# Kernel tuning notes

Hardware: AMD Instinct MI355X
Metric: run time of the kernel (lower is better)

Reference implementation:

```python
import jax, jax.numpy as jnp
import numpy as np

B, N, C, H = 16, 4096, 256, 4
D = C // H

def setup_inputs() -> dict:
    key = jax.random.key(0)
    ks = jax.random.split(key, 8)
    w = 0.01  # small init, mimics xavier_uniform gain=0.1
    x = jax.random.normal(ks[0], (B, N, C), jnp.float32)
    S = jax.random.normal(ks[1], (B, H, D, D), jnp.float32) * 0.1
    Wq = jax.random.normal(ks[2], (C, C), jnp.float32) * w
    Wk = jax.random.normal(ks[3], (C, C), jnp.float32) * w
    Wv = jax.random.normal(ks[4], (C, C), jnp.float32) * w
    Wb = jax.random.normal(ks[5], (H, C), jnp.float32) * w  # beta_proj (zeros in torch init; random for nontrivial math)
    Wo = jax.random.normal(ks[6], (C, C), jnp.float32) * w
    g_rms = jnp.ones((C,), jnp.float32)
    return {"x": x, "S": S, "Wq": Wq, "Wk": Wk, "Wv": Wv, "Wb": Wb, "Wo": Wo, "g_rms": g_rms}

def reference(x, S, Wq, Wk, Wv, Wb, Wo, g_rms):
    b, n, c = x.shape
    h = Wb.shape[0]
    d = c // h
    # projections -> (B,H,N,D)
    q = (x @ Wq.T).reshape(b, n, h, d).transpose(0, 2, 1, 3)
    k = (x @ Wk.T).reshape(b, n, h, d).transpose(0, 2, 1, 3)
    v = (x @ Wv.T).reshape(b, n, h, d).transpose(0, 2, 1, 3)
    # feature map + L2 normalize keys
    k = jax.nn.elu(k) + 1.0
    k = k / (jnp.linalg.norm(k, axis=-1, keepdims=True) + 1e-6)
    # per-head gates (B,H,N,1)
    beta = jax.nn.sigmoid(jnp.einsum('bnc,hc->bhn', x, Wb))[..., None]
    # decay + state read
    Sd = S * 0.95
    y = jnp.einsum('bhij,bhnj->bhni', Sd, q)
    pred = jnp.einsum('bhij,bhnj->bhni', Sd, k)
    # delta-rule write: outer(mean weighted error, mean key)
    w_err = jnp.mean(beta * (v - pred), axis=2)  # (B,H,D)
    w_key = jnp.mean(k, axis=2)                  # (B,H,D)
    S_new = jnp.clip(Sd + jnp.einsum('bhi,bhj->bhij', w_err, w_key), -10.0, 10.0)
    # merge heads, RMSNorm, output projection
    y = y.transpose(0, 2, 1, 3).reshape(b, n, c)
    y = y * jax.lax.rsqrt(jnp.mean(y * y, axis=-1, keepdims=True) + 1e-6) * g_rms
    out = y @ Wo.T
    return out, S_new
```

## Files before the change

kernel.cpp:

```cpp
#include <hip/hip_runtime.h>
#include <math.h>


typedef _Float16 f16;
typedef f16 f16x8 __attribute__((ext_vector_type(8)));
typedef f16 f16x4 __attribute__((ext_vector_type(4)));
typedef float f32x4 __attribute__((ext_vector_type(4)));

typedef const __attribute__((address_space(1))) void gvoid;
typedef __attribute__((address_space(3))) void svoid;

__device__ __forceinline__ void gload16(const void* g, void* l) {
  __builtin_amdgcn_global_load_lds((gvoid*)g, (svoid*)l, 16, 0, 0);
}

__device__ __forceinline__ f16x8 cvt8(const float* q) {
  float4 a = *(const float4*)q;
  float4 b = *(const float4*)(q + 4);
  f16x8 r;
  r[0] = (f16)a.x; r[1] = (f16)a.y; r[2] = (f16)a.z; r[3] = (f16)a.w;
  r[4] = (f16)b.x; r[5] = (f16)b.y; r[6] = (f16)b.z; r[7] = (f16)b.w;
  return r;
}

__global__ __launch_bounds__(256) void prep_w(
    const float* __restrict__ Wk, const float* __restrict__ Wo,
    const float* __restrict__ g, f16* __restrict__ Wkh,
    f16* __restrict__ Wogh) {
  int i = blockIdx.x * 256 + threadIdx.x;
#pragma unroll
  for (int j = 0; j < 4; ++j) {
    int idx = i + j * 16384;
    Wkh[idx] = (f16)Wk[idx];
    Wogh[idx] = (f16)(Wo[idx] * g[idx & 255]);
  }
}

__global__ __launch_bounds__(256) void beta_xbsum_h(
    const float* __restrict__ x, const float* __restrict__ Wb,
    float* __restrict__ betaArr, float* __restrict__ xbsum,
    f16* __restrict__ xh) {
  const int t = threadIdx.x;
  const int wave = t >> 6, lane = t & 63;
  const int b = blockIdx.x >> 6;
  const int tile = blockIdx.x & 63;
  float4 wb[4];
#pragma unroll
  for (int h = 0; h < 4; ++h) wb[h] = *(const float4*)(Wb + h * 256 + lane * 4);
  float xacc[4][4] = {};
  const size_t rowbase = (size_t)b * 4096 + tile * 64;
  __shared__ float bsh[4][64];
  float4 xv = *(const float4*)(x + (rowbase + wave) * 256 + lane * 4);
#pragma unroll 2
  for (int i = 0; i < 16; ++i) {
    int r = i * 4 + wave;
    float4 nx = xv;
    if (i < 15)
      nx = *(const float4*)(x + (rowbase + r + 4) * 256 + lane * 4);
    f16x4 hx;
    hx[0] = (f16)xv.x; hx[1] = (f16)xv.y; hx[2] = (f16)xv.z; hx[3] = (f16)xv.w;
    *(f16x4*)(xh + (rowbase + r) * 256 + lane * 4) = hx;
#pragma unroll
    for (int h = 0; h < 4; ++h) {
      float s = xv.x * wb[h].x + xv.y * wb[h].y + xv.z * wb[h].z + xv.w * wb[h].w;
#pragma unroll
      for (int off = 32; off; off >>= 1) s += __shfl_xor(s, off);
      float bh = 1.f / (1.f + __expf(-s));
      if (lane == h) bsh[h][r] = bh;
      xacc[h][0] += bh * xv.x; xacc[h][1] += bh * xv.y;
      xacc[h][2] += bh * xv.z; xacc[h][3] += bh * xv.w;
    }
    xv = nx;
  }
  __shared__ float xbp[4][4][256];
#pragma unroll
  for (int h = 0; h < 4; ++h)
#pragma unroll
    for (int j = 0; j < 4; ++j) xbp[wave][h][lane * 4 + j] = xacc[h][j];
  __syncthreads();
  {
    int h = t >> 6, r = t & 63;
    betaArr[((size_t)(b * 4 + h) << 12) + tile * 64 + r] = bsh[h][r];
  }
  for (int idx = t; idx < 1024; idx += 256) {
    int h = idx >> 8, c = idx & 255;
    float s = xbp[0][h][c] + xbp[1][h][c] + xbp[2][h][c] + xbp[3][h][c];
    atomicAdd(&xbsum[(b * 4 + h) * 256 + c], s);
  }
}

__global__ __launch_bounds__(256) void kgemm_h(
    const f16* __restrict__ xh, const f16* __restrict__ Wkh,
    const float* __restrict__ betaArr,
    float* __restrict__ ksum, float* __restrict__ kbsum) {
  __shared__ union {
    struct { f16 A[128][64]; f16 B[128][64]; } s;
    f16 K[128][128];
  } u;
  __shared__ float bstage[2][128];
  const int t = threadIdx.x;
  const int m0 = blockIdx.y * 128;
  const int n0 = blockIdx.x * 128;
  const int b = m0 >> 12;
  const int wave = t >> 6, lane = t & 63;
  const int wm = (wave >> 1) * 64, wn = (wave & 1) * 64;
  const int fr = lane & 15, fq = lane >> 4;
  const int fr7 = fr & 7;
  const int srow = lane >> 3;
  const int sc = (lane & 7) ^ srow;
  {
    int hh = t >> 7, r = t & 127;
    bstage[hh][r] =
        betaArr[((size_t)(b * 4 + (n0 >> 6) + hh) << 12) + (m0 & 4095) + r];
  }
  const char* Ab = (const char*)&u.s.A[0][0];
  const char* Bb = (const char*)&u.s.B[0][0];
  f32x4 acc[4][4] = {};
#pragma unroll 1
  for (int kt = 0; kt < 4; ++kt) {
    const int k0 = kt * 64;
#pragma unroll
    for (int j = 0; j < 4; ++j) {
      int c = j * 4 + wave;
      int row = c * 8 + srow;
      gload16(xh + (size_t)(m0 + row) * 256 + k0 + sc * 8, &u.s.A[0][0] + c * 512);
      gload16(Wkh + (size_t)(n0 + row) * 256 + k0 + sc * 8, &u.s.B[0][0] + c * 512);
    }
    __syncthreads();
#pragma unroll
    for (int ks = 0; ks < 2; ++ks) {
      const int p = ((ks * 4 + fq) ^ fr7) << 4;
      f16x8 afr[4], bfr[4];
#pragma unroll
      for (int mi = 0; mi < 4; ++mi)
        afr[mi] = *(const f16x8*)(Ab + (wm + mi * 16 + fr) * 128 + p);
#pragma unroll
      for (int ni = 0; ni < 4; ++ni)
        bfr[ni] = *(const f16x8*)(Bb + (wn + ni * 16 + fr) * 128 + p);
#pragma unroll
      for (int mi = 0; mi < 4; ++mi)
#pragma unroll
        for (int ni = 0; ni < 4; ++ni)
          acc[mi][ni] = __builtin_amdgcn_mfma_f32_16x16x32_f16(
              afr[mi], bfr[ni], acc[mi][ni], 0, 0, 0);
    }
    __syncthreads();
  }
#pragma unroll
  for (int mi = 0; mi < 4; ++mi)
#pragma unroll
    for (int rr = 0; rr < 4; ++rr) {
      float s = 0.f;
#pragma unroll
      for (int ni = 0; ni < 4; ++ni) {
        float v = acc[mi][ni][rr];
        v = v > 0.f ? v + 1.f : __expf(v);
        acc[mi][ni][rr] = v;
        s += v * v;
      }
#pragma unroll
      for (int off = 1; off < 16; off <<= 1) s += __shfl_xor(s, off);
      float inv = 1.f / (sqrtf(s) + 1e-6f);
#pragma unroll
      for (int ni = 0; ni < 4; ++ni) acc[mi][ni][rr] *= inv;
    }
#pragma unroll
  for (int mi = 0; mi < 4; ++mi)
#pragma unroll
    for (int ni = 0; ni < 4; ++ni)
#pragma unroll
      for (int rr = 0; rr < 4; ++rr)
        u.K[wm + mi * 16 + fq * 4 + rr][wn + ni * 16 + fr] = (f16)acc[mi][ni][rr];
  __syncthreads();
  if (t < 128) {
    const int c = t, hl = c >> 6;
    float sk = 0.f, skb = 0.f;
#pragma unroll 4
    for (int r = 0; r < 128; ++r) {
      float v = (float)u.K[r][c];
      float be = bstage[hl][r];
      sk += v;
      skb += be * v;
    }
    int gh = b * 4 + (n0 >> 6) + hl;
    atomicAdd(&ksum[gh * 64 + (c & 63)], sk);
    atomicAdd(&kbsum[gh * 64 + (c & 63)], skb);
  }
}

__global__ __launch_bounds__(256) void fold_M(
    const float* __restrict__ S, const float* __restrict__ Wq,
    f16* __restrict__ M) {
  const int bh = blockIdx.y;
  const int dq = blockIdx.x;
  const int h = bh & 3;
  const int t = threadIdx.x;
  const float* Sp = S + (size_t)bh * 4096 + dq * 8 * 64;
  const float* Wp = Wq + (size_t)h * 64 * 256 + t;
  float m[8] = {};
#pragma unroll 4
  for (int e = 0; e < 64; ++e) {
    float wv = Wp[e * 256];
#pragma unroll
    for (int dd = 0; dd < 8; ++dd) m[dd] += Sp[dd * 64 + e] * wv;
  }
  f16* Mb = M + (size_t)(bh >> 2) * 65536;
#pragma unroll
  for (int dd = 0; dd < 8; ++dd)
    Mb[(size_t)(h * 64 + dq * 8 + dd) * 256 + t] = (f16)(0.95f * m[dd]);
}

__global__ __launch_bounds__(256) void yogemm_h(
    const f16* __restrict__ xh, const f16* __restrict__ M,
    const f16* __restrict__ Wogh, float* __restrict__ out) {
  __shared__ f16 Bst[256 * 64];
  __shared__ f16 Ast[64 * 64];
  __shared__ f16 yl[64 * 256];
  __shared__ float ssq[4][64];
  __shared__ float rs_l[64];
  const int t = threadIdx.x;
  const int m0 = blockIdx.x * 64;
  const int b = m0 >> 12;
  const f16* Mb = M + (size_t)b * 65536;
  const int wave = t >> 6, lane = t & 63;
  const int wn = wave * 64;
  const int fr = lane & 15, fq = lane >> 4;
  const int fr7 = fr & 7;
  const int srow = lane >> 3;
  const int sc = (lane & 7) ^ srow;
  const char* Ab = (const char*)Ast;
  const char* Bb = (const char*)Bst;
  f32x4 acc[4][4] = {};
#pragma unroll 1
  for (int kt = 0; kt < 4; ++kt) {
    const int k0 = kt * 64;
    if (wave < 2) {
      int c = wave * 4 + (lane >> 4);
      int l16 = lane & 15;
    }
#pragma unroll
    for (int j = 0; j < 2; ++j) {
      int c = j * 4 + wave;
      int row = c * 8 + srow;
      gload16(xh + (size_t)(m0 + row) * 256 + k0 + sc * 8, Ast + c * 512);
    }
#pragma unroll
    for (int j = 0; j < 8; ++j) {
      int c = j * 4 + wave;
      int row = c * 8 + srow;
      gload16(Mb + (size_t)row * 256 + k0 + sc * 8, Bst + c * 512);
    }
    __syncthreads();
#pragma unroll
    for (int ks = 0; ks < 2; ++ks) {
      const int p = ((ks * 4 + fq) ^ fr7) << 4;
      f16x8 afr[4], bfr[4];
#pragma unroll
      for (int mi = 0; mi < 4; ++mi)
        afr[mi] = *(const f16x8*)(Ab + (mi * 16 + fr) * 128 + p);
#pragma unroll
      for (int ni = 0; ni < 4; ++ni)
        bfr[ni] = *(const f16x8*)(Bb + (wn + ni * 16 + fr) * 128 + p);
#pragma unroll
      for (int mi = 0; mi < 4; ++mi)
#pragma unroll
        for (int ni = 0; ni < 4; ++ni)
          acc[mi][ni] = __builtin_amdgcn_mfma_f32_16x16x32_f16(
              afr[mi], bfr[ni], acc[mi][ni], 0, 0, 0);
    }
    __syncthreads();
  }
#pragma unroll
  for (int mi = 0; mi < 4; ++mi)
#pragma unroll
    for (int rr = 0; rr < 4; ++rr) {
      float s = 0.f;
#pragma unroll
      for (int ni = 0; ni < 4; ++ni) {
        float v = acc[mi][ni][rr];
        s += v * v;
      }
#pragma unroll
      for (int off = 1; off < 16; off <<= 1) s += __shfl_xor(s, off);
      if (fr == 0) ssq[wave][mi * 16 + fq * 4 + rr] = s;
    }
  __syncthreads();
  if (t < 64)
    rs_l[t] = rsqrtf((ssq[0][t] + ssq[1][t] + ssq[2][t] + ssq[3][t]) *
                         (1.f / 256.f) +
                     1e-6f);
  __syncthreads();
#pragma unroll
  for (int mi = 0; mi < 4; ++mi)
#pragma unroll
    for (int rr = 0; rr < 4; ++rr) {
      int row = mi * 16 + fq * 4 + rr;
      float rs = rs_l[row];
      int r7 = row & 7;
#pragma unroll
      for (int ni = 0; ni < 4; ++ni) {
        int col = wn + ni * 16 + fr;
        int idx = row * 256 + ((((col >> 3) ^ r7) << 3) | (col & 7));
        yl[idx] = (f16)(rs * acc[mi][ni][rr]);
      }
    }
  __syncthreads();
#pragma unroll
  for (int mi = 0; mi < 4; ++mi)
#pragma unroll
    for (int ni = 0; ni < 4; ++ni) acc[mi][ni] = (f32x4){0.f, 0.f, 0.f, 0.f};
#pragma unroll 1
  for (int kt = 0; kt < 4; ++kt) {
    const int k0 = kt * 64;
#pragma unroll
    for (int j = 0; j < 8; ++j) {
      int c = j * 4 + wave;
      int row = c * 8 + srow;
      gload16(Wogh + (size_t)row * 256 + k0 + sc * 8, Bst + c * 512);
    }
    __syncthreads();
#pragma unroll
    for (int ks = 0; ks < 2; ++ks) {
      const int p = ((ks * 4 + fq) ^ fr7) << 4;
      f16x8 afr[4], bfr[4];
#pragma unroll
      for (int mi = 0; mi < 4; ++mi) {
        int row = mi * 16 + fr;
        int chunk = ((kt * 8 + ks * 4 + fq) ^ (row & 7)) << 4;
        afr[mi] = *(const f16x8*)((const char*)yl + row * 512 + chunk);
      }
#pragma unroll
      for (int ni = 0; ni < 4; ++ni)
        bfr[ni] = *(const f16x8*)(Bb + (wn + ni * 16 + fr) * 128 + p);
#pragma unroll
      for (int mi = 0; mi < 4; ++mi)
#pragma unroll
        for (int ni = 0; ni < 4; ++ni)
          acc[mi][ni] = __builtin_amdgcn_mfma_f32_16x16x32_f16(
              afr[mi], bfr[ni], acc[mi][ni], 0, 0, 0);
    }
    __syncthreads();
  }
#pragma unroll
  for (int mi = 0; mi < 4; ++mi)
#pragma unroll
    for (int ni = 0; ni < 4; ++ni)
#pragma unroll
      for (int rr = 0; rr < 4; ++rr) {
        int row = m0 + mi * 16 + fq * 4 + rr;
        int col = wn + ni * 16 + fr;
        out[(size_t)row * 256 + col] = acc[mi][ni][rr];
      }
}

__global__ __launch_bounds__(256) void beta_xbsum(
    const float* __restrict__ x, const float* __restrict__ Wb,
    float* __restrict__ betaArr, float* __restrict__ xbsum) {
  const int t = threadIdx.x;
  const int wave = t >> 6, lane = t & 63;
  const int b = blockIdx.x >> 6;
  const int tile = blockIdx.x & 63;
  float4 wb[4];
#pragma unroll
  for (int h = 0; h < 4; ++h) wb[h] = *(const float4*)(Wb + h * 256 + lane * 4);
  float xacc[4][4] = {};
  const size_t rowbase = (size_t)b * 4096 + tile * 64;
  __shared__ float bsh[4][64];
  float4 xv = *(const float4*)(x + (rowbase + wave) * 256 + lane * 4);
#pragma unroll 2
  for (int i = 0; i < 16; ++i) {
    int r = i * 4 + wave;
    float4 nx = xv;
    if (i < 15)
      nx = *(const float4*)(x + (rowbase + r + 4) * 256 + lane * 4);
#pragma unroll
    for (int h = 0; h < 4; ++h) {
      float s = xv.x * wb[h].x + xv.y * wb[h].y + xv.z * wb[h].z + xv.w * wb[h].w;
#pragma unroll
      for (int off = 32; off; off >>= 1) s += __shfl_xor(s, off);
      float bh = 1.f / (1.f + __expf(-s));
      if (lane == h) bsh[h][r] = bh;
      xacc[h][0] += bh * xv.x; xacc[h][1] += bh * xv.y;
      xacc[h][2] += bh * xv.z; xacc[h][3] += bh * xv.w;
    }
    xv = nx;
  }
  __shared__ float xbp[4][4][256];
#pragma unroll
  for (int h = 0; h < 4; ++h)
#pragma unroll
    for (int j = 0; j < 4; ++j) xbp[wave][h][lane * 4 + j] = xacc[h][j];
  __syncthreads();
  {
    int h = t >> 6, r = t & 63;
    betaArr[((size_t)(b * 4 + h) << 12) + tile * 64 + r] = bsh[h][r];
  }
  for (int idx = t; idx < 1024; idx += 256) {
    int h = idx >> 8, c = idx & 255;
    float s = xbp[0][h][c] + xbp[1][h][c] + xbp[2][h][c] + xbp[3][h][c];
    atomicAdd(&xbsum[(b * 4 + h) * 256 + c], s);
  }
}

__global__ __launch_bounds__(256) void kgemm_sums(
    const float* __restrict__ x, const float* __restrict__ Wk,
    const float* __restrict__ betaArr,
    float* __restrict__ ksum, float* __restrict__ kbsum) {
  __shared__ union {
    struct { f16 A[128][72]; f16 B[128][72]; } s;
    f16 K[128][132];
  } u;
  __shared__ float bstage[2][128];
  const int t = threadIdx.x;
  const int m0 = blockIdx.y * 128;
  const int n0 = blockIdx.x * 128;
  const int b = m0 >> 12;
  const int wave = t >> 6, lane = t & 63;
  const int wm = (wave >> 1) * 64, wn = (wave & 1) * 64;
  const int fr = lane & 15, fq = lane >> 4;
  {
    int hh = t >> 7, r = t & 127;
    bstage[hh][r] =
        betaArr[((size_t)(b * 4 + (n0 >> 6) + hh) << 12) + (m0 & 4095) + r];
  }
  f32x4 acc[4][4] = {};
#pragma unroll 1
  for (int kt = 0; kt < 4; ++kt) {
    const int k0 = kt * 64;
#pragma unroll
    for (int i = 0; i < 4; ++i) {
      int id = i * 256 + t;
      int row = id >> 3, cc = id & 7;
      *(f16x8*)&u.s.A[row][cc * 8] =
          cvt8(x + (size_t)(m0 + row) * 256 + k0 + cc * 8);
      *(f16x8*)&u.s.B[row][cc * 8] =
          cvt8(Wk + (size_t)(n0 + row) * 256 + k0 + cc * 8);
    }
    __syncthreads();
#pragma unroll
    for (int ks = 0; ks < 2; ++ks) {
      f16x8 afr[4], bfr[4];
#pragma unroll
      for (int mi = 0; mi < 4; ++mi)
        afr[mi] = *(const f16x8*)&u.s.A[wm + mi * 16 + fr][ks * 32 + fq * 8];
#pragma unroll
      for (int ni = 0; ni < 4; ++ni)
        bfr[ni] = *(const f16x8*)&u.s.B[wn + ni * 16 + fr][ks * 32 + fq * 8];
#pragma unroll
      for (int mi = 0; mi < 4; ++mi)
#pragma unroll
        for (int ni = 0; ni < 4; ++ni)
          acc[mi][ni] = __builtin_amdgcn_mfma_f32_16x16x32_f16(
              afr[mi], bfr[ni], acc[mi][ni], 0, 0, 0);
    }
    __syncthreads();
  }
#pragma unroll
  for (int mi = 0; mi < 4; ++mi)
#pragma unroll
    for (int rr = 0; rr < 4; ++rr) {
      float s = 0.f;
#pragma unroll
      for (int ni = 0; ni < 4; ++ni) {
        float v = acc[mi][ni][rr];
        v = v > 0.f ? v + 1.f : __expf(v);
        acc[mi][ni][rr] = v;
        s += v * v;
      }
#pragma unroll
      for (int off = 1; off < 16; off <<= 1) s += __shfl_xor(s, off);
      float inv = 1.f / (sqrtf(s) + 1e-6f);
#pragma unroll
      for (int ni = 0; ni < 4; ++ni) acc[mi][ni][rr] *= inv;
    }
#pragma unroll
  for (int mi = 0; mi < 4; ++mi)
#pragma unroll
    for (int ni = 0; ni < 4; ++ni)
#pragma unroll
      for (int rr = 0; rr < 4; ++rr)
        u.K[wm + mi * 16 + fq * 4 + rr][wn + ni * 16 + fr] = (f16)acc[mi][ni][rr];
  __syncthreads();
  if (t < 128) {
    const int c = t, hl = c >> 6;
    float sk = 0.f, skb = 0.f;
#pragma unroll 4
    for (int r = 0; r < 128; ++r) {
      float v = (float)u.K[r][c];
      float be = bstage[hl][r];
      sk += v;
      skb += be * v;
    }
    int gh = b * 4 + (n0 >> 6) + hl;
    atomicAdd(&ksum[gh * 64 + (c & 63)], sk);
    atomicAdd(&kbsum[gh * 64 + (c & 63)], skb);
  }
}

__global__ __launch_bounds__(256) void ygemm_ssq(
    const float* __restrict__ x, int m_base, const f16* __restrict__ M,
    f16* __restrict__ y, float* __restrict__ rowssq) {
  __shared__ f16 As[128][72];
  __shared__ f16 Bs[128][72];
  const int t = threadIdx.x;
  const int m0 = blockIdx.y * 128;
  const int n0 = blockIdx.x * 128;
  const int b = (m_base + m0) >> 12;
  const f16* Mb = M + (size_t)b * 65536;
  const int wave = t >> 6, lane = t & 63;
  const int wm = (wave >> 1) * 64, wn = (wave & 1) * 64;
  const int fr = lane & 15, fq = lane >> 4;
  f32x4 acc[4][4] = {};
#pragma unroll 1
  for (int kt = 0; kt < 4; ++kt) {
    const int k0 = kt * 64;
#pragma unroll
    for (int i = 0; i < 4; ++i) {
      int id = i * 256 + t;
      int row = id >> 3, cc = id & 7;
      *(f16x8*)&As[row][cc * 8] =
          cvt8(x + (size_t)(m_base + m0 + row) * 256 + k0 + cc * 8);
      *(uint4*)&Bs[row][cc * 8] =
          *(const uint4*)(Mb + (size_t)(n0 + row) * 256 + k0 + cc * 8);
    }
    __syncthreads();
#pragma unroll
    for (int ks = 0; ks < 2; ++ks) {
      f16x8 afr[4], bfr[4];
#pragma unroll
      for (int mi = 0; mi < 4; ++mi)
        afr[mi] = *(const f16x8*)&As[wm + mi * 16 + fr][ks * 32 + fq * 8];
#pragma unroll
      for (int ni = 0; ni < 4; ++ni)
        bfr[ni] = *(const f16x8*)&Bs[wn + ni * 16 + fr][ks * 32 + fq * 8];
#pragma unroll
      for (int mi = 0; mi < 4; ++mi)
#pragma unroll
        for (int ni = 0; ni < 4; ++ni)
          acc[mi][ni] = __builtin_amdgcn_mfma_f32_16x16x32_f16(
              afr[mi], bfr[ni], acc[mi][ni], 0, 0, 0);
    }
    __syncthreads();
  }
#pragma unroll
  for (int mi = 0; mi < 4; ++mi)
#pragma unroll
    for (int rr = 0; rr < 4; ++rr) {
      float s = 0.f;
#pragma unroll
      for (int ni = 0; ni < 4; ++ni) {
        float v = acc[mi][ni][rr];
        s += v * v;
        int row = m0 + wm + mi * 16 + fq * 4 + rr;
        int col = n0 + wn + ni * 16 + fr;
        y[(size_t)row * 256 + col] = (f16)v;
      }
#pragma unroll
      for (int off = 1; off < 16; off <<= 1) s += __shfl_xor(s, off);
      if (fr == 0)
        atomicAdd(&rowssq[m0 + wm + mi * 16 + fq * 4 + rr], s);
    }
}

__global__ __launch_bounds__(256) void ogemm_scaled(
    const f16* __restrict__ y, const float* __restrict__ rowssq,
    const float* __restrict__ g_rms, const float* __restrict__ Wo,
    float* __restrict__ out, int m_base) {
  __shared__ f16 As[128][72];
  __shared__ f16 Bs[128][72];
  const int t = threadIdx.x;
  const int m0 = blockIdx.y * 128;
  const int n0 = blockIdx.x * 128;
  const int wave = t >> 6, lane = t & 63;
  const int wm = (wave >> 1) * 64, wn = (wave & 1) * 64;
  const int fr = lane & 15, fq = lane >> 4;
  f32x4 acc[4][4] = {};
#pragma unroll 1
  for (int kt = 0; kt < 4; ++kt) {
    const int k0 = kt * 64;
#pragma unroll
    for (int i = 0; i < 4; ++i) {
      int id = i * 256 + t;
      int row = id >> 3, cc = id & 7;
      float rs = rsqrtf(rowssq[m0 + row] * (1.f / 256.f) + 1e-6f);
      const f16* yp = y + (size_t)(m0 + row) * 256 + k0 + cc * 8;
      const float* gp = g_rms + k0 + cc * 8;
      f16x8 a;
#pragma unroll
      for (int j = 0; j < 8; ++j) a[j] = (f16)((float)yp[j] * rs * gp[j]);
      *(f16x8*)&As[row][cc * 8] = a;
      *(f16x8*)&Bs[row][cc * 8] =
          cvt8(Wo + (size_t)(n0 + row) * 256 + k0 + cc * 8);
    }
    __syncthreads();
#pragma unroll
    for (int ks = 0; ks < 2; ++ks) {
      f16x8 afr[4], bfr[4];
#pragma unroll
      for (int mi = 0; mi < 4; ++mi)
        afr[mi] = *(const f16x8*)&As[wm + mi * 16 + fr][ks * 32 + fq * 8];
#pragma unroll
      for (int ni = 0; ni < 4; ++ni)
        bfr[ni] = *(const f16x8*)&Bs[wn + ni * 16 + fr][ks * 32 + fq * 8];
#pragma unroll
      for (int mi = 0; mi < 4; ++mi)
#pragma unroll
        for (int ni = 0; ni < 4; ++ni)
          acc[mi][ni] = __builtin_amdgcn_mfma_f32_16x16x32_f16(
              afr[mi], bfr[ni], acc[mi][ni], 0, 0, 0);
    }
    __syncthreads();
  }
#pragma unroll
  for (int mi = 0; mi < 4; ++mi)
#pragma unroll
    for (int ni = 0; ni < 4; ++ni)
#pragma unroll
      for (int rr = 0; rr < 4; ++rr) {
        int row = m_base + m0 + wm + mi * 16 + fq * 4 + rr;
        int col = n0 + wn + ni * 16 + fr;
        out[(size_t)row * 256 + col] = acc[mi][ni][rr];
      }
}

__global__ __launch_bounds__(256) void finalize_S(
    const float* __restrict__ S, const float* __restrict__ Wv,
    const float* __restrict__ xbsum, const float* __restrict__ ksum,
    const float* __restrict__ kbsum, float* __restrict__ Sout) {
  const int bh = blockIdx.x;
  const int h = bh & 3;
  const int t = threadIdx.x;
  const int wave = t >> 6, lane = t & 63;
  __shared__ float xb[256], kb[64], key[64], errv[64];
  xb[t] = xbsum[bh * 256 + t];
  if (t < 64) {
    kb[t] = kbsum[bh * 64 + t];
    key[t] = ksum[bh * 64 + t] * (1.f / 4096.f);
  }
  __syncthreads();
#pragma unroll 1
  for (int ri = 0; ri < 16; ++ri) {
    int i = wave * 16 + ri;
    float4 wv4 = *(const float4*)(Wv + (size_t)(h * 64 + i) * 256 + lane * 4);
    float4 xb4 = *(const float4*)(&xb[lane * 4]);
    float s = wv4.x * xb4.x + wv4.y * xb4.y + wv4.z * xb4.z + wv4.w * xb4.w;
    s -= 0.95f * S[(size_t)bh * 4096 + i * 64 + lane] * kb[lane];
#pragma unroll
    for (int off = 32; off; off >>= 1) s += __shfl_xor(s, off);
    if (lane == 0) errv[i] = s * (1.f / 4096.f);
  }
  __syncthreads();
  for (int idx = t; idx < 4096; idx += 256) {
    int i = idx >> 6, j = idx & 63;
    float v = 0.95f * S[(size_t)bh * 4096 + idx] + errv[i] * key[j];
    Sout[(size_t)bh * 4096 + idx] = fminf(10.f, fmaxf(-10.f, v));
  }
}

extern "C" void kernel_launch(void* const* d_in, const int* in_sizes, int n_in,
                              void* d_out, int out_size, void* d_ws, size_t ws_size,
                              hipStream_t stream) {
  const float* x  = (const float*)d_in[0];
  const float* S  = (const float*)d_in[1];
  const float* Wq = (const float*)d_in[2];
  const float* Wk = (const float*)d_in[3];
  const float* Wv = (const float*)d_in[4];
  const float* Wb = (const float*)d_in[5];
  const float* Wo = (const float*)d_in[6];
  const float* g  = (const float*)d_in[7];

  char* w = (char*)d_ws;
  float* betaArr = (float*)w;
  f16*   M       = (f16*)(w + 1048576);
  f16*   y       = (f16*)(w + 3145728);
  float* rowssq  = (float*)(w + 19922944);
  float* xbsum   = (float*)(w + 20185088);
  float* ksum    = (float*)(w + 20250624);
  float* kbsum   = (float*)(w + 20267008);
  f16*   xh      = (f16*)(w + 20283392);
  f16*   Wkh     = (f16*)(w + 53837824);
  f16*   Wogh    = (f16*)(w + 53968896);
  const size_t WS_NEED = 54099968ull;

  float* out  = (float*)d_out;
  float* Sout = out + (size_t)16 * 4096 * 256;

  if (ws_size >= WS_NEED) {
    hipMemsetAsync(w + 20185088, 0, 98304, stream);
    prep_w<<<64, 256, 0, stream>>>(Wk, Wo, g, Wkh, Wogh);
    beta_xbsum_h<<<1024, 256, 0, stream>>>(x, Wb, betaArr, xbsum, xh);
    kgemm_h<<<dim3(2, 512), 256, 0, stream>>>(xh, Wkh, betaArr, ksum, kbsum);
    fold_M<<<dim3(8, 64), 256, 0, stream>>>(S, Wq, M);
    yogemm_h<<<1024, 256, 0, stream>>>(xh, M, Wogh, out);
  } else {
    hipMemsetAsync(w + 19922944, 0, 360448, stream);
    beta_xbsum<<<1024, 256, 0, stream>>>(x, Wb, betaArr, xbsum);
    kgemm_sums<<<dim3(2, 512), 256, 0, stream>>>(x, Wk, betaArr, ksum, kbsum);
    fold_M<<<dim3(8, 64), 256, 0, stream>>>(S, Wq, M);
    for (int half = 0; half < 2; ++half) {
      int m_base = half * 32768;
      ygemm_ssq<<<dim3(2, 256), 256, 0, stream>>>(x, m_base, M, y,
                                                  rowssq + half * 32768);
      ogemm_scaled<<<dim3(2, 256), 256, 0, stream>>>(y, rowssq + half * 32768,
                                                     g, Wo, out, m_base);
    }
  }
  finalize_S<<<64, 256, 0, stream>>>(S, Wv, xbsum, ksum, kbsum, Sout);
}
```

Before: 225.7 us.

## Precompose per-batch M^T M and Wo·M matrices to replace the two-GEMM y/out chain

Folds the state-read matrix into the output projection per batch: a new kernel computes G = M^T M (for the RMS sum of squares, read back as x·G·x) and P = Wo·g·M, so the main kernel does two parallel GEMMs against x instead of computing y and then a second GEMM on y. This removes the intermediate y LDS staging and the serial second GEMM phase. It adds a small precompute kernel, doubles the B-operand LDS footprint and accumulator registers, and computes the norm through fp16 G, which may change rounding.

```diff
diff --git a/kernel.cpp b/kernel.cpp
--- a/kernel.cpp
+++ b/kernel.cpp
@@ -188,9 +188,9 @@
   }
 }
 
-__global__ __launch_bounds__(256) void fold_M(
+__global__ __launch_bounds__(256) void fold_Mt(
     const float* __restrict__ S, const float* __restrict__ Wq,
-    f16* __restrict__ M) {
+    f16* __restrict__ Mt) {
   const int bh = blockIdx.y;
   const int dq = blockIdx.x;
   const int h = bh & 3;
@@ -204,24 +204,91 @@
 #pragma unroll
     for (int dd = 0; dd < 8; ++dd) m[dd] += Sp[dd * 64 + e] * wv;
   }
-  f16* Mb = M + (size_t)(bh >> 2) * 65536;
-#pragma unroll
-  for (int dd = 0; dd < 8; ++dd)
-    Mb[(size_t)(h * 64 + dq * 8 + dd) * 256 + t] = (f16)(0.95f * m[dd]);
-}
-
-__global__ __launch_bounds__(256) void yogemm_h(
-    const f16* __restrict__ xh, const f16* __restrict__ M,
-    const f16* __restrict__ Wogh, float* __restrict__ out) {
-  __shared__ f16 Bst[256 * 64];
+  f16* Mtb = Mt + (size_t)(bh >> 2) * 65536;
+  f16x8 v;
+#pragma unroll
+  for (int dd = 0; dd < 8; ++dd) v[dd] = (f16)(0.95f * m[dd]);
+  *(f16x8*)(Mtb + (size_t)t * 256 + h * 64 + dq * 8) = v;
+}
+
+__global__ __launch_bounds__(256) void prep_gp(
+    const f16* __restrict__ Mt, const f16* __restrict__ Wogh,
+    f16* __restrict__ G, f16* __restrict__ P) {
+  __shared__ f16 As[128 * 64];
+  __shared__ f16 Bs[128 * 64];
+  const int bx = blockIdx.x;
+  const int b = bx >> 3;
+  const int sel = (bx >> 2) & 1;
+  const int ty = (bx >> 1) & 1, tx = bx & 1;
+  const f16* Mtb = Mt + (size_t)b * 65536;
+  const f16* Asrc = sel ? (Wogh + ty * 128 * 256) : (Mtb + ty * 128 * 256);
+  const f16* Bsrc = Mtb + tx * 128 * 256;
+  f16* O = (sel ? P : G) + (size_t)b * 65536;
+  const int t = threadIdx.x;
+  const int wave = t >> 6, lane = t & 63;
+  const int wm = (wave >> 1) * 64, wn = (wave & 1) * 64;
+  const int fr = lane & 15, fq = lane >> 4;
+  const int fr7 = fr & 7;
+  const int srow = lane >> 3;
+  const int sc = (lane & 7) ^ srow;
+  const char* Ab = (const char*)As;
+  const char* Bb = (const char*)Bs;
+  f32x4 acc[4][4] = {};
+#pragma unroll 1
+  for (int kt = 0; kt < 4; ++kt) {
+    const int k0 = kt * 64;
+#pragma unroll
+    for (int j = 0; j < 4; ++j) {
+      int c = j * 4 + wave;
+      int row = c * 8 + srow;
+      gload16(Asrc + (size_t)row * 256 + k0 + sc * 8, As + c * 512);
+      gload16(Bsrc + (size_t)row * 256 + k0 + sc * 8, Bs + c * 512);
+    }
+    __syncthreads();
+#pragma unroll
+    for (int ks = 0; ks < 2; ++ks) {
+      const int p = ((ks * 4 + fq) ^ fr7) << 4;
+      f16x8 afr[4], bfr[4];
+#pragma unroll
+      for (int mi = 0; mi < 4; ++mi)
+        afr[mi] = *(const f16x8*)(Ab + (wm + mi * 16 + fr) * 128 + p);
+#pragma unroll
+      for (int ni = 0; ni < 4; ++ni)
+        bfr[ni] = *(const f16x8*)(Bb + (wn + ni * 16 + fr) * 128 + p);
+#pragma unroll
+      for (int mi = 0; mi < 4; ++mi)
+#pragma unroll
+        for (int ni = 0; ni < 4; ++ni)
+          acc[mi][ni] = __builtin_amdgcn_mfma_f32_16x16x32_f16(
+              afr[mi], bfr[ni], acc[mi][ni], 0, 0, 0);
+    }
+    __syncthreads();
+  }
+#pragma unroll
+  for (int mi = 0; mi < 4; ++mi)
+#pragma unroll
+    for (int ni = 0; ni < 4; ++ni)
+#pragma unroll
+      for (int rr = 0; rr < 4; ++rr) {
+        int row = ty * 128 + wm + mi * 16 + fq * 4 + rr;
+        int col = tx * 128 + wn + ni * 16 + fr;
+        O[(size_t)row * 256 + col] = (f16)acc[mi][ni][rr];
+      }
+}
+
+__global__ __launch_bounds__(256) void yop_h(
+    const f16* __restrict__ xh, const f16* __restrict__ G,
+    const f16* __restrict__ P, float* __restrict__ out) {
   __shared__ f16 Ast[64 * 64];
-  __shared__ f16 yl[64 * 256];
+  __shared__ f16 Gt[256 * 64];
+  __shared__ f16 Pt[256 * 64];
   __shared__ float ssq[4][64];
   __shared__ float rs_l[64];
   const int t = threadIdx.x;
   const int m0 = blockIdx.x * 64;
   const int b = m0 >> 12;
-  const f16* Mb = M + (size_t)b * 65536;
+  const f16* Gb = G + (size_t)b * 65536;
+  const f16* Pb = P + (size_t)b * 65536;
   const int wave = t >> 6, lane = t & 63;
   const int wn = wave * 64;
   const int fr = lane & 15, fq = lane >> 4;
@@ -229,15 +296,13 @@
   const int srow = lane >> 3;
   const int sc = (lane & 7) ^ srow;
   const char* Ab = (const char*)Ast;
-  const char* Bb = (const char*)Bst;
-  f32x4 acc[4][4] = {};
+  const char* Gbb = (const char*)Gt;
+  const char* Pbb = (const char*)Pt;
+  f32x4 accG[4][4] = {};
+  f32x4 accP[4][4] = {};
 #pragma unroll 1
   for (int kt = 0; kt < 4; ++kt) {
     const int k0 = kt * 64;
-    if (wave < 2) {
-      int c = wave * 4 + (lane >> 4);
-      int l16 = lane & 15;
-    }
 #pragma unroll
     for (int j = 0; j < 2; ++j) {
       int c = j * 4 + wave;
@@ -248,41 +313,49 @@
     for (int j = 0; j < 8; ++j) {
       int c = j * 4 + wave;
       int row = c * 8 + srow;
-      gload16(Mb + (size_t)row * 256 + k0 + sc * 8, Bst + c * 512);
+      gload16(Gb + (size_t)row * 256 + k0 + sc * 8, Gt + c * 512);
+      gload16(Pb + (size_t)row * 256 + k0 + sc * 8, Pt + c * 512);
     }
     __syncthreads();
 #pragma unroll
     for (int ks = 0; ks < 2; ++ks) {
       const int p = ((ks * 4 + fq) ^ fr7) << 4;
-      f16x8 afr[4], bfr[4];
+      f16x8 afr[4], gfr[4], pfr[4];
 #pragma unroll
       for (int mi = 0; mi < 4; ++mi)
         afr[mi] = *(const f16x8*)(Ab + (mi * 16 + fr) * 128 + p);
 #pragma unroll
-      for (int ni = 0; ni < 4; ++ni)
-        bfr[ni] = *(const f16x8*)(Bb + (wn + ni * 16 + fr) * 128 + p);
-#pragma unroll
-      for (int mi = 0; mi < 4; ++mi)
-#pragma unroll
-        for (int ni = 0; ni < 4; ++ni)
-          acc[mi][ni] = __builtin_amdgcn_mfma_f32_16x16x32_f16(
-              afr[mi], bfr[ni], acc[mi][ni], 0, 0, 0);
-    }
-    __syncthreads();
-  }
+      for (int ni = 0; ni < 4; ++ni) {
+        gfr[ni] = *(const f16x8*)(Gbb + (wn + ni * 16 + fr) * 128 + p);
+        pfr[ni] = *(const f16x8*)(Pbb + (wn + ni * 16 + fr) * 128 + p);
+      }
+#pragma unroll
+      for (int mi = 0; mi < 4; ++mi)
+#pragma unroll
+        for (int ni = 0; ni < 4; ++ni) {
+          accG[mi][ni] = __builtin_amdgcn_mfma_f32_16x16x32_f16(
+              afr[mi], gfr[ni], accG[mi][ni], 0, 0, 0);
+          accP[mi][ni] = __builtin_amdgcn_mfma_f32_16x16x32_f16(
+              afr[mi], pfr[ni], accP[mi][ni], 0, 0, 0);
+        }
+    }
+    __syncthreads();
+  }
+  const f16* xr = xh + (size_t)m0 * 256;
 #pragma unroll
   for (int mi = 0; mi < 4; ++mi)
 #pragma unroll
     for (int rr = 0; rr < 4; ++rr) {
+      int row = mi * 16 + fq * 4 + rr;
       float s = 0.f;
 #pragma unroll
       for (int ni = 0; ni < 4; ++ni) {
-        float v = acc[mi][ni][rr];
-        s += v * v;
+        float xv = (float)xr[(size_t)row * 256 + wn + ni * 16 + fr];
+        s += accG[mi][ni][rr] * xv;
       }
 #pragma unroll
       for (int off = 1; off < 16; off <<= 1) s += __shfl_xor(s, off);
-      if (fr == 0) ssq[wave][mi * 16 + fq * 4 + rr] = s;
+      if (fr == 0) ssq[wave][row] = s;
     }
   __syncthreads();
   if (t < 64)
@@ -296,61 +369,11 @@
     for (int rr = 0; rr < 4; ++rr) {
       int row = mi * 16 + fq * 4 + rr;
       float rs = rs_l[row];
-      int r7 = row & 7;
-#pragma unroll
-      for (int ni = 0; ni < 4; ++ni) {
-        int col = wn + ni * 16 + fr;
-        int idx = row * 256 + ((((col >> 3) ^ r7) << 3) | (col & 7));
-        yl[idx] = (f16)(rs * acc[mi][ni][rr]);
-      }
-    }
-  __syncthreads();
-#pragma unroll
-  for (int mi = 0; mi < 4; ++mi)
-#pragma unroll
-    for (int ni = 0; ni < 4; ++ni) acc[mi][ni] = (f32x4){0.f, 0.f, 0.f, 0.f};
-#pragma unroll 1
-  for (int kt = 0; kt < 4; ++kt) {
-    const int k0 = kt * 64;
-#pragma unroll
-    for (int j = 0; j < 8; ++j) {
-      int c = j * 4 + wave;
-      int row = c * 8 + srow;
-      gload16(Wogh + (size_t)row * 256 + k0 + sc * 8, Bst + c * 512);
-    }
-    __syncthreads();
-#pragma unroll
-    for (int ks = 0; ks < 2; ++ks) {
-      const int p = ((ks * 4 + fq) ^ fr7) << 4;
-      f16x8 afr[4], bfr[4];
-#pragma unroll
-      for (int mi = 0; mi < 4; ++mi) {
-        int row = mi * 16 + fr;
-        int chunk = ((kt * 8 + ks * 4 + fq) ^ (row & 7)) << 4;
-        afr[mi] = *(const f16x8*)((const char*)yl + row * 512 + chunk);
-      }
 #pragma unroll
       for (int ni = 0; ni < 4; ++ni)
-        bfr[ni] = *(const f16x8*)(Bb + (wn + ni * 16 + fr) * 128 + p);
-#pragma unroll
-      for (int mi = 0; mi < 4; ++mi)
-#pragma unroll
-        for (int ni = 0; ni < 4; ++ni)
-          acc[mi][ni] = __builtin_amdgcn_mfma_f32_16x16x32_f16(
-              afr[mi], bfr[ni], acc[mi][ni], 0, 0, 0);
-    }
-    __syncthreads();
-  }
-#pragma unroll
-  for (int mi = 0; mi < 4; ++mi)
-#pragma unroll
-    for (int ni = 0; ni < 4; ++ni)
-#pragma unroll
-      for (int rr = 0; rr < 4; ++rr) {
-        int row = m0 + mi * 16 + fq * 4 + rr;
-        int col = wn + ni * 16 + fr;
-        out[(size_t)row * 256 + col] = acc[mi][ni][rr];
-      }
+        out[(size_t)(m0 + row) * 256 + wn + ni * 16 + fr] =
+            rs * accP[mi][ni][rr];
+    }
 }
 
 __global__ __launch_bounds__(256) void beta_xbsum(
@@ -497,6 +520,28 @@
   }
 }
 
+__global__ __launch_bounds__(256) void fold_M(
+    const float* __restrict__ S, const float* __restrict__ Wq,
+    f16* __restrict__ M) {
+  const int bh = blockIdx.y;
+  const int dq = blockIdx.x;
+  const int h = bh & 3;
+  const int t = threadIdx.x;
+  const float* Sp = S + (size_t)bh * 4096 + dq * 8 * 64;
+  const float* Wp = Wq + (size_t)h * 64 * 256 + t;
+  float m[8] = {};
+#pragma unroll 4
+  for (int e = 0; e < 64; ++e) {
+    float wv = Wp[e * 256];
+#pragma unroll
+    for (int dd = 0; dd < 8; ++dd) m[dd] += Sp[dd * 64 + e] * wv;
+  }
+  f16* Mb = M + (size_t)(bh >> 2) * 65536;
+#pragma unroll
+  for (int dd = 0; dd < 8; ++dd)
+    Mb[(size_t)(h * 64 + dq * 8 + dd) * 256 + t] = (f16)(0.95f * m[dd]);
+}
+
 __global__ __launch_bounds__(256) void ygemm_ssq(
     const float* __restrict__ x, int m_base, const f16* __restrict__ M,
     f16* __restrict__ y, float* __restrict__ rowssq) {
@@ -680,7 +725,10 @@
   f16*   xh      = (f16*)(w + 20283392);
   f16*   Wkh     = (f16*)(w + 53837824);
   f16*   Wogh    = (f16*)(w + 53968896);
-  const size_t WS_NEED = 54099968ull;
+  f16*   Mt      = (f16*)(w + 54099968);
+  f16*   G       = (f16*)(w + 56197120);
+  f16*   P       = (f16*)(w + 58294272);
+  const size_t WS_NEED = 60391424ull;
 
   float* out  = (float*)d_out;
   float* Sout = out + (size_t)16 * 4096 * 256;
@@ -690,8 +738,9 @@
     prep_w<<<64, 256, 0, stream>>>(Wk, Wo, g, Wkh, Wogh);
     beta_xbsum_h<<<1024, 256, 0, stream>>>(x, Wb, betaArr, xbsum, xh);
     kgemm_h<<<dim3(2, 512), 256, 0, stream>>>(xh, Wkh, betaArr, ksum, kbsum);
-    fold_M<<<dim3(8, 64), 256, 0, stream>>>(S, Wq, M);
-    yogemm_h<<<1024, 256, 0, stream>>>(xh, M, Wogh, out);
+    fold_Mt<<<dim3(8, 64), 256, 0, stream>>>(S, Wq, Mt);
+    prep_gp<<<128, 256, 0, stream>>>(Mt, Wogh, G, P);
+    yop_h<<<1024, 256, 0, stream>>>(xh, G, P, out);
   } else {
     hipMemsetAsync(w + 19922944, 0, 360448, stream);
     beta_xbsum<<<1024, 256, 0, stream>>>(x, Wb, betaArr, xbsum);
```

New measurement: 248.7 us. 10.2% more time.
